# Kernel optimization log

Hardware: AMD Instinct MI355X
Metric: run time of the kernel (lower is better)

Reference implementation:

```python
import jax, jax.numpy as jnp
import numpy as np

D_MODEL = 2048
N_HEADS = 16
HEAD_DIM = D_MODEL // N_HEADS


def setup_inputs() -> dict:
    key = jax.random.key(0)
    ks = jax.random.split(key, 9)
    s = 0.02
    B, S = 4, 2048
    return {
        "x": jax.random.normal(ks[0], (B, S, D_MODEL), dtype=jnp.float32),
        "Wq": jax.random.normal(ks[1], (D_MODEL, D_MODEL), dtype=jnp.float32) * s,
        "bq": jnp.zeros((D_MODEL,), dtype=jnp.float32),
        "Wk": jax.random.normal(ks[2], (D_MODEL, D_MODEL), dtype=jnp.float32) * s,
        "bk": jnp.zeros((D_MODEL,), dtype=jnp.float32),
        "Wv": jax.random.normal(ks[3], (D_MODEL, D_MODEL), dtype=jnp.float32) * s,
        "bv": jnp.zeros((D_MODEL,), dtype=jnp.float32),
        "Wo": jax.random.normal(ks[4], (D_MODEL, D_MODEL), dtype=jnp.float32) * s,
        "bo": jnp.zeros((D_MODEL,), dtype=jnp.float32),
    }


def reference(x, Wq, bq, Wk, bk, Wv, bv, Wo, bo):
    B, S, _ = x.shape
    scale = jnp.asarray(np.sqrt(HEAD_DIM), dtype=x.dtype)

    def split_heads(t):  # [B,S,D] -> [B,H,S,hd]
        return t.reshape(B, S, N_HEADS, HEAD_DIM).transpose(0, 2, 1, 3)

    q = split_heads(x @ Wq + bq)
    k = split_heads(x @ Wk + bk)
    v = split_heads(x @ Wv + bv)

    # scores: [B,H,S,S]
    attn = jnp.einsum('bhqd,bhkd->bhqk', q, k) / scale
    kv_len = S
    causal = jnp.triu(jnp.ones((S, kv_len), dtype=bool), k=kv_len - S + 1)
    attn = jnp.where(causal[None, None], -jnp.inf, attn)
    attn = jax.nn.softmax(attn, axis=-1)
    # dropout is identity (p=0 / eval mode)
    out = jnp.einsum('bhqk,bhkd->bhqd', attn, v)
    out = out.transpose(0, 2, 1, 3).reshape(B, S, D_MODEL)
    return out @ Wo + bo
```

## Files before the change

kernel.cpp:

```cpp
#include <hip/hip_runtime.h>
#include <hip/hip_bf16.h>

#define DEV __device__ __forceinline__

typedef __bf16 bf16_t;
typedef __bf16 bf16x8 __attribute__((ext_vector_type(8)));
typedef __bf16 bf16x4 __attribute__((ext_vector_type(4)));
typedef float f32x4 __attribute__((ext_vector_type(4)));
typedef float f32x16 __attribute__((ext_vector_type(16)));
typedef unsigned int u32;
typedef unsigned short u16;
typedef u32 u32x4 __attribute__((ext_vector_type(4)));

constexpr int D_MODEL = 2048;
constexpr int SEQ = 2048;
constexpr int BATCH = 4;
constexpr int N_HEADS = 16;
constexpr int HEAD_DIM = 128;
constexpr int TOK = BATCH * SEQ;

DEV void gload_lds16(const void* g, void* l) {
  __builtin_amdgcn_global_load_lds(
      (const __attribute__((address_space(1))) unsigned int*)g,
      (__attribute__((address_space(3))) unsigned int*)l, 16, 0, 0);
}

DEV float fast_exp2(float x) {
#if __has_builtin(__builtin_amdgcn_exp2f)
  return __builtin_amdgcn_exp2f(x);
#else
  return exp2f(x);
#endif
}

DEV u32 pack2(float lo, float hi) {
  u16 a = __builtin_bit_cast(u16, (bf16_t)lo);
  u16 b = __builtin_bit_cast(u16, (bf16_t)hi);
  return (u32)a | ((u32)b << 16);
}

#define MFMA16(a, b, c) __builtin_amdgcn_mfma_f32_16x16x32_bf16((a), (b), (c), 0, 0, 0)
#define MFMA32(a, b, c) __builtin_amdgcn_mfma_f32_32x32x16_bf16((a), (b), (c), 0, 0, 0)

__global__ void k_prep(const float* __restrict__ x, bf16_t* __restrict__ xb,
                       const float* __restrict__ Wq, const float* __restrict__ Wk,
                       const float* __restrict__ Wv, const float* __restrict__ Wo,
                       bf16_t* __restrict__ WqkvT, bf16_t* __restrict__ WoT) {
  const int z = blockIdx.z;
  if (z < 4) {
    __shared__ float t[32][33];
    const float* W = z == 0 ? Wq : z == 1 ? Wk : z == 2 ? Wv : Wo;
    bf16_t* Wt = z < 3 ? WqkvT + (size_t)z * D_MODEL * D_MODEL : WoT;
    int k0 = blockIdx.x * 32, n0 = blockIdx.y * 32;
    int tx = threadIdx.x, ty = threadIdx.y;
#pragma unroll
    for (int r = ty; r < 32; r += 8)
      t[r][tx] = W[(size_t)(k0 + r) * D_MODEL + n0 + tx];
    __syncthreads();
#pragma unroll
    for (int r = ty; r < 32; r += 8)
      Wt[(size_t)(n0 + r) * D_MODEL + k0 + tx] = (bf16_t)t[tx][r];
  } else {
    const int n4 = TOK * D_MODEL / 4;
    const int tid = threadIdx.y * 32 + threadIdx.x;
    int i = (blockIdx.y * 64 + blockIdx.x) * 256 + tid;
    const int stride = 64 * 64 * 256;
    for (; i < n4; i += stride) {
      float4 v = ((const float4*)x)[i];
      bf16x4 o;
      o[0] = (bf16_t)v.x; o[1] = (bf16_t)v.y; o[2] = (bf16_t)v.z; o[3] = (bf16_t)v.w;
      ((bf16x4*)xb)[i] = o;
    }
  }
}

template <int MODE>
__global__ __launch_bounds__(512, 2) void k_gemm256(const bf16_t* __restrict__ A,
                                                    const bf16_t* __restrict__ Bt,
                                                    const float* __restrict__ b0p,
                                                    const float* __restrict__ b1p,
                                                    const float* __restrict__ b2p,
                                                    void* __restrict__ o0,
                                                    void* __restrict__ o1,
                                                    void* __restrict__ o2) {
  constexpr int K = D_MODEL;
  constexpr int NTOT = (MODE == 0) ? 3 * D_MODEL : D_MODEL;
  constexpr int NT = K / 64;
  constexpr int NBM = TOK / 256;
  __shared__ __attribute__((aligned(16))) bf16_t sh[2][2][2][8192];

  const int bid = blockIdx.x;
  const int cpx = gridDim.x >> 3;
  const int swz = (bid & 7) * cpx + (bid >> 3);
  const int grp = swz / (NBM * 4);
  const int rem = swz % (NBM * 4);
  const int bm = rem >> 2;
  const int bn = grp * 4 + (rem & 3);

  const int tid = threadIdx.x;
  const int lane = tid & 63;
  const int w = tid >> 6;
  const int wm = w >> 2, wn = w & 3;
  const int lr = lane & 15, lg = lane >> 4;

  const bf16_t* Agl[2];
  const bf16_t* Bgl[2];
  int ldsg[2];
#pragma unroll
  for (int l = 0; l < 2; ++l) {
    int g = l * 512 + tid;
    int r = g >> 2, c = g & 3;
    int csw = c ^ ((r ^ (r >> 2)) & 3);
    Agl[l] = A + (size_t)(bm * 256 + r) * K + csw * 8;
    Bgl[l] = Bt + (size_t)(bn * 256 + r) * K + csw * 8;
    ldsg[l] = g * 8;
  }

  auto SA = [&](int buf, int t, int kh) {
    const int off = t * 64 + kh * 32;
#pragma unroll
    for (int l = 0; l < 2; ++l) gload_lds16(Agl[l] + off, &sh[buf][0][kh][ldsg[l]]);
  };
  auto SB = [&](int buf, int t, int kh) {
    const int off = t * 64 + kh * 32;
#pragma unroll
    for (int l = 0; l < 2; ++l) gload_lds16(Bgl[l] + off, &sh[buf][1][kh][ldsg[l]]);
  };

  int offA[8], offB[4];
  const int cx = lg ^ ((lr ^ (lr >> 2)) & 3);
#pragma unroll
  for (int i = 0; i < 8; ++i) offA[i] = (wm * 128 + i * 16 + lr) * 32 + cx * 8;
#pragma unroll
  for (int j = 0; j < 4; ++j) offB[j] = (wn * 64 + j * 16 + lr) * 32 + cx * 8;

  f32x4 acc[8][4] = {};
  bf16x8 af[8], bf_[4];

  SA(0, 0, 0); SB(0, 0, 0); SA(0, 0, 1); SB(0, 0, 1);

#define MFMA_ROW(i)                                  \
  acc[i][0] = MFMA16(af[i], bf_[0], acc[i][0]);      \
  acc[i][1] = MFMA16(af[i], bf_[1], acc[i][1]);      \
  acc[i][2] = MFMA16(af[i], bf_[2], acc[i][2]);      \
  acc[i][3] = MFMA16(af[i], bf_[3], acc[i][3]);

  for (int t = 0; t < NT; ++t) {
    const int cur = t & 1, nxt = cur ^ 1;
    const int t1 = (t + 1 < NT) ? t + 1 : NT - 1;
#pragma unroll
    for (int kh = 0; kh < 2; ++kh) {
      asm volatile("s_waitcnt vmcnt(4)" ::: "memory");
      __builtin_amdgcn_s_barrier();
#pragma unroll
      for (int j = 0; j < 4; ++j) bf_[j] = *(const bf16x8*)&sh[cur][1][kh][offB[j]];
#pragma unroll
      for (int i = 0; i < 8; ++i) af[i] = *(const bf16x8*)&sh[cur][0][kh][offA[i]];
      SA(nxt, t1, kh);
      SB(nxt, t1, kh);
      __builtin_amdgcn_s_setprio(1);
      asm volatile("s_waitcnt lgkmcnt(6)" ::: "memory");
      __builtin_amdgcn_sched_barrier(0);
      MFMA_ROW(0) MFMA_ROW(1)
      asm volatile("s_waitcnt lgkmcnt(4)" ::: "memory");
      __builtin_amdgcn_sched_barrier(0);
      MFMA_ROW(2) MFMA_ROW(3)
      asm volatile("s_waitcnt lgkmcnt(2)" ::: "memory");
      __builtin_amdgcn_sched_barrier(0);
      MFMA_ROW(4) MFMA_ROW(5)
      asm volatile("s_waitcnt lgkmcnt(0)" ::: "memory");
      __builtin_amdgcn_sched_barrier(0);
      MFMA_ROW(6) MFMA_ROW(7)
      __builtin_amdgcn_s_setprio(0);
    }
  }
#undef MFMA_ROW

  asm volatile("s_waitcnt vmcnt(0) lgkmcnt(0)" ::: "memory");

  const float CQ = 0.12751949848078418f;
#pragma unroll
  for (int i = 0; i < 8; ++i) {
    const int row = bm * 256 + wm * 128 + i * 16 + lg * 4;
#pragma unroll
    for (int jn = 0; jn < 4; ++jn) {
      const int col = bn * 256 + wn * 64 + jn * 16 + lr;
      if (MODE == 1) {
        const float bv = b0p[col];
        float* Cf = (float*)o0;
#pragma unroll
        for (int j = 0; j < 4; ++j)
          Cf[(size_t)(row + j) * D_MODEL + col] = acc[i][jn][j] + bv;
      } else {
        const int sel = col >> 11, cl = col & 2047;
        const float bv = (sel == 0 ? b0p : sel == 1 ? b1p : b2p)[cl];
        if (sel < 2) {
          const float scl = (sel == 0) ? CQ : 1.0f;
          bf16_t* dst = (bf16_t*)(sel == 0 ? o0 : o1);
#pragma unroll
          for (int j = 0; j < 4; ++j)
            dst[(size_t)(row + j) * D_MODEL + cl] = (bf16_t)((acc[i][jn][j] + bv) * scl);
        } else {
          const int bb2 = row >> 11, s = row & 2047;
          bf16x4 ov;
#pragma unroll
          for (int j = 0; j < 4; ++j) ov[j] = (bf16_t)(acc[i][jn][j] + bv);
          bf16_t* Vt = (bf16_t*)o2;
          *(bf16x4*)(Vt + (((size_t)(bb2 * 16 + (cl >> 7))) * 128 + (cl & 127)) * 2048 + s) = ov;
        }
      }
    }
  }
}

__global__ __launch_bounds__(256, 3) void k_attn(const bf16_t* __restrict__ Q,
                                                 const bf16_t* __restrict__ K,
                                                 const bf16_t* __restrict__ Vt,
                                                 bf16_t* __restrict__ AO) {
  const int fid = blockIdx.x;
  const int qb = 15 - (fid >> 6);
  const int bh = fid & 63;
  const int b = bh >> 4, h = bh & 15;
  const int w = threadIdx.x >> 6, lane = threadIdx.x & 63;
  const int l31 = lane & 31, hl = lane >> 5;
  const int nt = 4 * qb + 4;

  __shared__ __attribute__((aligned(16))) bf16_t Ks[3][32 * 128];
  __shared__ __attribute__((aligned(16))) bf16_t Vs[3][128 * 32];

  const bf16_t* kbase = K + (size_t)(b * SEQ) * D_MODEL + h * HEAD_DIM;
  const bf16_t* vtbase = Vt + (size_t)bh * HEAD_DIM * SEQ;

  auto STAGE = [&](int buf, int kt) {
    const int tt = threadIdx.x;
#pragma unroll
    for (int p = 0; p < 2; ++p) {
      int g = p * 256 + tt;
      int r = g >> 4, c = g & 15;
      gload_lds16(kbase + (size_t)(kt * 32 + r) * D_MODEL + ((c ^ (r & 7)) * 8),
                  &Ks[buf][(size_t)(g & ~63) * 8]);
    }
#pragma unroll
    for (int p = 0; p < 2; ++p) {
      int g = p * 256 + tt;
      int r = g >> 2, c = g & 3;
      gload_lds16(vtbase + (size_t)r * SEQ + kt * 32 + ((c ^ ((r ^ (r >> 2)) & 3)) * 8),
                  &Vs[buf][(size_t)(g & ~63) * 8]);
    }
  };

  const int qw0 = qb * 128 + w * 32;
  const int qa = qw0 + l31;

  const bf16_t* qp = Q + (size_t)(b * SEQ + qa) * D_MODEL + h * HEAD_DIM + hl * 8;
  bf16x8 qf[8];
#pragma unroll
  for (int step = 0; step < 8; ++step) qf[step] = *(const bf16x8*)(qp + step * 16);

  f32x16 oacc[4];
#pragma unroll
  for (int db = 0; db < 4; ++db)
#pragma unroll
    for (int r = 0; r < 16; ++r) oacc[db][r] = 0.f;
  float m = -1e30f, lsum = 0.f;

  STAGE(0, 0);
  STAGE(1, 1);

  int cur = 0, stg = 2;
  for (int kt = 0; kt < nt; ++kt) {
    if (kt < nt - 1) {
      asm volatile("s_waitcnt vmcnt(4)" ::: "memory");
    } else {
      asm volatile("s_waitcnt vmcnt(0)" ::: "memory");
    }
    __builtin_amdgcn_s_barrier();
    asm volatile("" ::: "memory");
    if (kt + 2 < nt) STAGE(stg, kt + 2);

    if (kt * 32 < qw0 + 32) {
      f32x16 sacc;
#pragma unroll
      for (int r = 0; r < 16; ++r) sacc[r] = 0.f;
      const bf16_t* kr = &Ks[cur][l31 * 128];
      const int rx = l31 & 7;
      __builtin_amdgcn_s_setprio(1);
#pragma unroll
      for (int step = 0; step < 8; ++step) {
        bf16x8 kf = *(const bf16x8*)(kr + (((step * 2 + hl) ^ rx) * 8));
        sacc = MFMA32(kf, qf[step], sacc);
      }
      __builtin_amdgcn_s_setprio(0);

      const bool domask = (kt * 32 + 31 > qw0);
      if (domask) {
#pragma unroll
        for (int r = 0; r < 16; ++r) {
          int kv = kt * 32 + 4 * hl + (r & 3) + 8 * (r >> 2);
          if (kv > qa) sacc[r] = -1e30f;
        }
      }
      float mx8[8];
#pragma unroll
      for (int r = 0; r < 8; ++r) mx8[r] = fmaxf(sacc[r], sacc[r + 8]);
#pragma unroll
      for (int r = 0; r < 4; ++r) mx8[r] = fmaxf(mx8[r], mx8[r + 4]);
      float tm = fmaxf(fmaxf(mx8[0], mx8[1]), fmaxf(mx8[2], mx8[3]));
      tm = fmaxf(tm, __shfl_xor(tm, 32));

      if (!__all(tm <= m + 11.5f)) {
        const float mn = fmaxf(m, tm);
        const float al = fast_exp2(m - mn);
        lsum *= al;
#pragma unroll
        for (int db = 0; db < 4; ++db)
#pragma unroll
          for (int r = 0; r < 16; ++r) oacc[db][r] *= al;
        m = mn;
      }

#pragma unroll
      for (int r = 0; r < 16; ++r) sacc[r] = fast_exp2(sacc[r] - m);
      float sm8[8];
#pragma unroll
      for (int r = 0; r < 8; ++r) sm8[r] = sacc[r] + sacc[r + 8];
#pragma unroll
      for (int r = 0; r < 4; ++r) sm8[r] = sm8[r] + sm8[r + 4];
      float ls = (sm8[0] + sm8[1]) + (sm8[2] + sm8[3]);
      lsum += ls + __shfl_xor(ls, 32);

      bf16x8 pb[2];
#pragma unroll
      for (int ck = 0; ck < 2; ++ck) {
        u32 a0 = pack2(sacc[8 * ck + 0], sacc[8 * ck + 1]);
        u32 a1 = pack2(sacc[8 * ck + 2], sacc[8 * ck + 3]);
        u32 b0 = pack2(sacc[8 * ck + 4], sacc[8 * ck + 5]);
        u32 b1 = pack2(sacc[8 * ck + 6], sacc[8 * ck + 7]);
        u32 send0 = hl ? a0 : b0, send1 = hl ? a1 : b1;
        u32 keep0 = hl ? b0 : a0, keep1 = hl ? b1 : a1;
        u32 r0 = __shfl_xor(send0, 32), r1 = __shfl_xor(send1, 32);
        u32x4 fv;
        fv[0] = hl ? r0 : keep0;
        fv[1] = hl ? r1 : keep1;
        fv[2] = hl ? keep0 : r0;
        fv[3] = hl ? keep1 : r1;
        pb[ck] = __builtin_bit_cast(bf16x8, fv);
      }

      __builtin_amdgcn_s_setprio(1);
#pragma unroll
      for (int db = 0; db < 4; ++db) {
        const int vrow = db * 32 + l31;
        const bf16_t* vr = &Vs[cur][vrow * 32];
        const int vx = (vrow ^ (vrow >> 2)) & 3;
#pragma unroll
        for (int ck = 0; ck < 2; ++ck) {
          bf16x8 vf = *(const bf16x8*)(vr + (((ck * 2 + hl) ^ vx) * 8));
          oacc[db] = MFMA32(vf, pb[ck], oacc[db]);
        }
      }
      __builtin_amdgcn_s_setprio(0);
    }

    cur = (cur == 2) ? 0 : cur + 1;
    stg = (stg == 2) ? 0 : stg + 1;
  }

  const float inv = 1.f / lsum;
  bf16_t* ao = AO + (size_t)(b * SEQ + qa) * D_MODEL + h * HEAD_DIM;
#pragma unroll
  for (int db = 0; db < 4; ++db)
#pragma unroll
    for (int g = 0; g < 4; ++g) {
      bf16x4 ov;
#pragma unroll
      for (int j = 0; j < 4; ++j) ov[j] = (bf16_t)(oacc[db][4 * g + j] * inv);
      *(bf16x4*)(ao + db * 32 + 8 * g + 4 * hl) = ov;
    }
}

extern "C" void kernel_launch(void* const* d_in, const int* in_sizes, int n_in,
                              void* d_out, int out_size, void* d_ws, size_t ws_size,
                              hipStream_t stream) {
  const float* x  = (const float*)d_in[0];
  const float* Wq = (const float*)d_in[1];
  const float* bq = (const float*)d_in[2];
  const float* Wk = (const float*)d_in[3];
  const float* bk = (const float*)d_in[4];
  const float* Wv = (const float*)d_in[5];
  const float* bv = (const float*)d_in[6];
  const float* Wo = (const float*)d_in[7];
  const float* bo = (const float*)d_in[8];

  const size_t SZ_X = (size_t)TOK * D_MODEL * sizeof(bf16_t);
  const size_t SZ_W = (size_t)D_MODEL * D_MODEL * sizeof(bf16_t);

  char* p = (char*)d_ws;
  bf16_t* xb    = (bf16_t*)p;                     p += SZ_X;
  bf16_t* WqkvT = (bf16_t*)p;                     p += 3 * SZ_W;
  bf16_t* WoT   = (bf16_t*)p;                     p += SZ_W;
  bf16_t* Qm    = (bf16_t*)p;                     p += SZ_X;
  bf16_t* Km    = (bf16_t*)p;                     p += SZ_X;
  bf16_t* Vt    = (bf16_t*)p;                     p += SZ_X;
  bf16_t* AO    = xb;

  k_prep<<<dim3(64, 64, 5), dim3(32, 8), 0, stream>>>(x, xb, Wq, Wk, Wv, Wo, WqkvT, WoT);

  const int gqkv = (TOK / 256) * (3 * D_MODEL / 256);
  k_gemm256<0><<<gqkv, 512, 0, stream>>>(xb, WqkvT, bq, bk, bv, Qm, Km, Vt);

  k_attn<<<1024, 256, 0, stream>>>(Qm, Km, Vt, AO);

  const int go = (TOK / 256) * (D_MODEL / 256);
  k_gemm256<1><<<go, 512, 0, stream>>>(AO, WoT, bo, nullptr, nullptr, d_out, nullptr, nullptr);
}
```

Measured before the change: 405.3 us.

## Load GEMM B operand directly from global into registers, skipping LDS staging

```diff
diff --git a/kernel.cpp b/kernel.cpp
--- a/kernel.cpp
+++ b/kernel.cpp
@@ -87,7 +87,7 @@
   constexpr int NTOT = (MODE == 0) ? 3 * D_MODEL : D_MODEL;
   constexpr int NT = K / 64;
   constexpr int NBM = TOK / 256;
-  __shared__ __attribute__((aligned(16))) bf16_t sh[2][2][2][8192];
+  __shared__ __attribute__((aligned(16))) bf16_t shA[2][2][8192];
 
   const int bid = blockIdx.x;
   const int cpx = gridDim.x >> 3;
@@ -104,7 +104,6 @@
   const int lr = lane & 15, lg = lane >> 4;
 
   const bf16_t* Agl[2];
-  const bf16_t* Bgl[2];
   int ldsg[2];
 #pragma unroll
   for (int l = 0; l < 2; ++l) {
@@ -112,68 +111,71 @@
     int r = g >> 2, c = g & 3;
     int csw = c ^ ((r ^ (r >> 2)) & 3);
     Agl[l] = A + (size_t)(bm * 256 + r) * K + csw * 8;
-    Bgl[l] = Bt + (size_t)(bn * 256 + r) * K + csw * 8;
     ldsg[l] = g * 8;
   }
 
   auto SA = [&](int buf, int t, int kh) {
     const int off = t * 64 + kh * 32;
 #pragma unroll
-    for (int l = 0; l < 2; ++l) gload_lds16(Agl[l] + off, &sh[buf][0][kh][ldsg[l]]);
+    for (int l = 0; l < 2; ++l) gload_lds16(Agl[l] + off, &shA[buf][kh][ldsg[l]]);
   };
-  auto SB = [&](int buf, int t, int kh) {
-    const int off = t * 64 + kh * 32;
-#pragma unroll
-    for (int l = 0; l < 2; ++l) gload_lds16(Bgl[l] + off, &sh[buf][1][kh][ldsg[l]]);
-  };
-
-  int offA[8], offB[4];
+
+  const bf16_t* Bdir = Bt + (size_t)(bn * 256 + wn * 64 + lr) * K + lg * 8;
+
+  int offA[8];
   const int cx = lg ^ ((lr ^ (lr >> 2)) & 3);
 #pragma unroll
   for (int i = 0; i < 8; ++i) offA[i] = (wm * 128 + i * 16 + lr) * 32 + cx * 8;
-#pragma unroll
-  for (int j = 0; j < 4; ++j) offB[j] = (wn * 64 + j * 16 + lr) * 32 + cx * 8;
 
   f32x4 acc[8][4] = {};
-  bf16x8 af[8], bf_[4];
-
-  SA(0, 0, 0); SB(0, 0, 0); SA(0, 0, 1); SB(0, 0, 1);
-
-#define MFMA_ROW(i)                                  \
-  acc[i][0] = MFMA16(af[i], bf_[0], acc[i][0]);      \
-  acc[i][1] = MFMA16(af[i], bf_[1], acc[i][1]);      \
-  acc[i][2] = MFMA16(af[i], bf_[2], acc[i][2]);      \
-  acc[i][3] = MFMA16(af[i], bf_[3], acc[i][3]);
+  bf16x8 af[8], bfA[4], bfB[4];
+
+  SA(0, 0, 0); SA(0, 0, 1);
+  __builtin_amdgcn_sched_barrier(0);
+#pragma unroll
+  for (int j = 0; j < 4; ++j) bfA[j] = *(const bf16x8*)(Bdir + (size_t)j * 16 * K);
+  asm volatile("s_waitcnt vmcnt(0)" ::: "memory");
+  __builtin_amdgcn_s_barrier();
+
+#define MFMA_ROW(i, BF)                              \
+  acc[i][0] = MFMA16(af[i], BF[0], acc[i][0]);       \
+  acc[i][1] = MFMA16(af[i], BF[1], acc[i][1]);       \
+  acc[i][2] = MFMA16(af[i], BF[2], acc[i][2]);       \
+  acc[i][3] = MFMA16(af[i], BF[3], acc[i][3]);
+
+#define PHASE(CUR, KH, BFC, BFN, NOFF, SAb, SAt, SAkh)                         \
+  asm volatile("s_waitcnt vmcnt(2)" ::: "memory");                             \
+  __builtin_amdgcn_s_barrier();                                                \
+  _Pragma("unroll")                                                            \
+  for (int i = 0; i < 8; ++i) af[i] = *(const bf16x8*)&shA[CUR][KH][offA[i]];  \
+  __builtin_amdgcn_sched_barrier(0);                                           \
+  _Pragma("unroll")                                                            \
+  for (int j = 0; j < 4; ++j)                                                  \
+    BFN[j] = *(const bf16x8*)(Bdir + (size_t)j * 16 * K + (NOFF));             \
+  __builtin_amdgcn_sched_barrier(0);                                           \
+  SA(SAb, SAt, SAkh);                                                          \
+  __builtin_amdgcn_s_setprio(1);                                               \
+  asm volatile("s_waitcnt lgkmcnt(6)" ::: "memory");                           \
+  __builtin_amdgcn_sched_barrier(0);                                           \
+  MFMA_ROW(0, BFC) MFMA_ROW(1, BFC)                                            \
+  asm volatile("s_waitcnt lgkmcnt(4)" ::: "memory");                           \
+  __builtin_amdgcn_sched_barrier(0);                                           \
+  MFMA_ROW(2, BFC) MFMA_ROW(3, BFC)                                            \
+  asm volatile("s_waitcnt lgkmcnt(2)" ::: "memory");                           \
+  __builtin_amdgcn_sched_barrier(0);                                           \
+  MFMA_ROW(4, BFC) MFMA_ROW(5, BFC)                                            \
+  asm volatile("s_waitcnt lgkmcnt(0)" ::: "memory");                           \
+  __builtin_amdgcn_sched_barrier(0);                                           \
+  MFMA_ROW(6, BFC) MFMA_ROW(7, BFC)                                            \
+  __builtin_amdgcn_s_setprio(0);
 
   for (int t = 0; t < NT; ++t) {
     const int cur = t & 1, nxt = cur ^ 1;
     const int t1 = (t + 1 < NT) ? t + 1 : NT - 1;
-#pragma unroll
-    for (int kh = 0; kh < 2; ++kh) {
-      asm volatile("s_waitcnt vmcnt(4)" ::: "memory");
-      __builtin_amdgcn_s_barrier();
-#pragma unroll
-      for (int j = 0; j < 4; ++j) bf_[j] = *(const bf16x8*)&sh[cur][1][kh][offB[j]];
-#pragma unroll
-      for (int i = 0; i < 8; ++i) af[i] = *(const bf16x8*)&sh[cur][0][kh][offA[i]];
-      SA(nxt, t1, kh);
-      SB(nxt, t1, kh);
-      __builtin_amdgcn_s_setprio(1);
-      asm volatile("s_waitcnt lgkmcnt(6)" ::: "memory");
-      __builtin_amdgcn_sched_barrier(0);
-      MFMA_ROW(0) MFMA_ROW(1)
-      asm volatile("s_waitcnt lgkmcnt(4)" ::: "memory");
-      __builtin_amdgcn_sched_barrier(0);
-      MFMA_ROW(2) MFMA_ROW(3)
-      asm volatile("s_waitcnt lgkmcnt(2)" ::: "memory");
-      __builtin_amdgcn_sched_barrier(0);
-      MFMA_ROW(4) MFMA_ROW(5)
-      asm volatile("s_waitcnt lgkmcnt(0)" ::: "memory");
-      __builtin_amdgcn_sched_barrier(0);
-      MFMA_ROW(6) MFMA_ROW(7)
-      __builtin_amdgcn_s_setprio(0);
-    }
+    PHASE(cur, 0, bfA, bfB, t * 64 + 32, nxt, t1, 0)
+    PHASE(cur, 1, bfB, bfA, (size_t)t1 * 64, nxt, t1, 1)
   }
+#undef PHASE
 #undef MFMA_ROW
 
   asm volatile("s_waitcnt vmcnt(0) lgkmcnt(0)" ::: "memory");
```

After: 546.8 us. +34.9%, slower.
